# Kernel optimization log

Hardware: AMD Instinct MI355X
Metric: run time of the kernel (lower is better)

Reference implementation:

```python
import jax, jax.numpy as jnp
import numpy as np

H = 64
V = 50257
B = 32
L = 4096
LN_EPS = 1e-5
DELTA_EPS = 1e-6


def setup_inputs() -> dict:
    key = jax.random.key(0)
    ks = jax.random.split(key, 10)
    s = 0.02
    return {
        "seq": jax.random.randint(ks[0], (B, L), 0, V),
        "read_pos": -1,
        "embed": jax.random.normal(ks[1], (V, H), jnp.float32) * s,
        "w1": jax.random.normal(ks[2], (H, 2 * H), jnp.float32) * s,
        "b1": jnp.zeros((2 * H,), jnp.float32),
        "w2": jax.random.normal(ks[3], (2 * H, H), jnp.float32) * s,
        "b2": jnp.zeros((H,), jnp.float32),
        "ln_g": jnp.ones((H,), jnp.float32),
        "ln_b": jnp.zeros((H,), jnp.float32),
        "rp_w": jax.random.normal(ks[4], (H, H), jnp.float32) * s,
        "rp_b": jnp.zeros((H,), jnp.float32),
        "out_w": jax.random.normal(ks[5], (H, V), jnp.float32) * s,
        "out_b": jnp.zeros((V,), jnp.float32),
    }


def _encoder(seq, embed, w1, b1, w2, b2, ln_g, ln_b):
    e = embed[seq]  # [B, L, H]
    f = jnp.maximum(e @ w1 + b1, 0.0) @ w2 + b2  # FFN
    x = e + f
    mu = jnp.mean(x, axis=-1, keepdims=True)
    var = jnp.mean((x - mu) ** 2, axis=-1, keepdims=True)
    return (x - mu) * jax.lax.rsqrt(var + LN_EPS) * ln_g + ln_b


def _delta_memory(h_all):
    # Strictly sequential delta-rule fast-weight update over t = 0..L-2.
    Bs, Ls, Hs = h_all.shape
    keys = jnp.transpose(h_all[:, : Ls - 1, :], (1, 0, 2))  # [L-1, B, H]

    def step(M, k):
        vp = jnp.einsum('bij,bj->bi', M, k)  # M @ k
        u = k - vp / (jnp.sum(k * k, axis=-1, keepdims=True) + DELTA_EPS)
        M = M + u[:, :, None] * k[:, None, :]  # outer product update
        return M, None

    M0 = jnp.zeros((Bs, Hs, Hs), h_all.dtype)
    M, _ = jax.lax.scan(step, M0, keys)
    return M


def reference(seq, read_pos, embed, w1, b1, w2, b2, ln_g, ln_b, rp_w, rp_b, out_w, out_b):
    h_all = _encoder(seq, embed, w1, b1, w2, b2, ln_g, ln_b)  # [B, L, H]
    M = _delta_memory(h_all)  # [B, H, H]
    q = h_all[:, read_pos, :]  # [B, H]
    r = jnp.einsum('bij,bj->bi', M, q)
    return (r @ rp_w + rp_b) @ out_w + out_b  # [B, V]
```

## Files before the change

### kernel.cpp

```cpp
#include <hip/hip_runtime.h>

#define HH 64
#define VV 50257
#define BB 32
#define LL 4096

constexpr float LN_EPS_F = 1e-5f;
constexpr float DELTA_EPS_F = 1e-6f;

constexpr int CS = 64;
constexpr int NG = LL / CS;

typedef float f32x4 __attribute__((ext_vector_type(4)));
typedef float f32x2 __attribute__((ext_vector_type(2)));
typedef short bf16x8 __attribute__((ext_vector_type(8)));
union U16x8 { uint4 u; bf16x8 v; unsigned short s[8]; };

__device__ __forceinline__ unsigned short f2bf(float f) {
  union { float f; unsigned u; } v; v.f = f;
  unsigned r = v.u + 0x7fff + ((v.u >> 16) & 1);
  return (unsigned short)(r >> 16);
}

__device__ __forceinline__ unsigned cvt_pk_bf16(float a, float b) {
  unsigned r;
  asm("v_cvt_pk_bf16_f32 %0, %1, %2" : "=v"(r) : "v"(a), "v"(b));
  return r;
}

__device__ __forceinline__ void split2(float a, float b, unsigned& hp, unsigned& lp) {
  hp = cvt_pk_bf16(a, b);
  float ha = __uint_as_float(hp << 16);
  float hb = __uint_as_float(hp & 0xffff0000u);
  lp = cvt_pk_bf16(a - ha, b - hb);
}

template <int CTRL>
__device__ __forceinline__ float dpp_add(float x) {
  int t = __builtin_amdgcn_update_dpp(0, __float_as_int(x), CTRL, 0xF, 0xF, true);
  return x + __int_as_float(t);
}

__device__ __forceinline__ float wave_sum_lane63(float x) {
  x = dpp_add<0x111>(x);
  x = dpp_add<0x112>(x);
  x = dpp_add<0x114>(x);
  x = dpp_add<0x118>(x);
  x = dpp_add<0x142>(x);
  x = dpp_add<0x143>(x);
  return x;
}

__device__ __forceinline__ float readlane_f(float x, int lane) {
  return __int_as_float(__builtin_amdgcn_readlane(__float_as_int(x), lane));
}

__global__ __launch_bounds__(256) void prep_kernel(
    const float* __restrict__ w1, const float* __restrict__ w2,
    unsigned short* __restrict__ w1b, unsigned short* __restrict__ w2b) {
  int i = blockIdx.x * 256 + threadIdx.x;
  if (i < 8192) {
    int jj = i >> 6, h = i & 63;
    w1b[i] = f2bf(w1[h * 128 + jj]);
  } else {
    int k = i - 8192;
    int h = k >> 7, jj = k & 127;
    w2b[k] = f2bf(w2[jj * 64 + h]);
  }
}

__global__ __launch_bounds__(64, 1) void encoder_kernel(
    const int* __restrict__ seq, const float* __restrict__ embed,
    const unsigned short* __restrict__ w1b, const float* __restrict__ b1,
    const unsigned short* __restrict__ w2b, const float* __restrict__ b2,
    const float* __restrict__ ln_g, const float* __restrict__ ln_b,
    float* __restrict__ h_all, float* __restrict__ beta) {
  __shared__ __align__(16) char pool[16640];
  unsigned short (*e_l)[72] = reinterpret_cast<unsigned short (*)[72]>(pool);
  unsigned short (*chunk)[40] = reinterpret_cast<unsigned short (*)[40]>(pool + 9216);
  float (*x_l)[65] = reinterpret_cast<float (*)[65]>(pool);
  __shared__ float2 gb_l[64];
  __shared__ float b1_l[128], b2_l[64];

  int lane = threadIdx.x;
  int q = lane >> 4, l = lane & 15;
  int base = blockIdx.x * 64;
  int s = seq[base + lane];

  {
    const float4* ep = reinterpret_cast<const float4*>(embed + (size_t)s * HH);
#pragma unroll
    for (int i = 0; i < 8; ++i) {
      float4 va = ep[2 * i], vb = ep[2 * i + 1];
      uint4 u;
      u.x = cvt_pk_bf16(va.x, va.y);
      u.y = cvt_pk_bf16(va.z, va.w);
      u.z = cvt_pk_bf16(vb.x, vb.y);
      u.w = cvt_pk_bf16(vb.z, vb.w);
      *(uint4*)&e_l[lane][8 * i] = u;
    }
  }
  gb_l[lane] = make_float2(ln_g[lane], ln_b[lane]);
  b1_l[lane] = b1[lane];
  b1_l[64 + lane] = b1[64 + lane];
  b2_l[lane] = b2[lane];

  bf16x8 af1[8][2];
#pragma unroll
  for (int mi = 0; mi < 8; ++mi)
#pragma unroll
    for (int ks = 0; ks < 2; ++ks) {
      U16x8 t;
      t.u = *(const uint4*)(w1b + (mi * 16 + l) * 64 + ks * 32 + q * 8);
      af1[mi][ks] = t.v;
    }

  __syncthreads();

  f32x4 acc1[8][4];
#pragma unroll
  for (int mi = 0; mi < 8; ++mi)
#pragma unroll
    for (int nt = 0; nt < 4; ++nt) acc1[mi][nt] = (f32x4){0.f, 0.f, 0.f, 0.f};

#pragma unroll
  for (int ks = 0; ks < 2; ++ks) {
    bf16x8 bfr[4];
#pragma unroll
    for (int nt = 0; nt < 4; ++nt) {
      U16x8 t;
      t.u = *(const uint4*)&e_l[nt * 16 + l][ks * 32 + q * 8];
      bfr[nt] = t.v;
    }
#pragma unroll
    for (int mi = 0; mi < 8; ++mi)
#pragma unroll
      for (int nt = 0; nt < 4; ++nt)
        acc1[mi][nt] = __builtin_amdgcn_mfma_f32_16x16x32_bf16(
            af1[mi][ks], bfr[nt], acc1[mi][nt], 0, 0, 0);
  }

  bf16x8 bf2[4][4];
#pragma unroll
  for (int nt = 0; nt < 4; ++nt)
#pragma unroll
    for (int ks = 0; ks < 4; ++ks) {
      U16x8 t;
      t.u = *(const uint4*)(w2b + (nt * 16 + l) * 128 + ks * 32 + q * 8);
      bf2[nt][ks] = t.v;
    }

  f32x4 acc2[4][4];
#pragma unroll
  for (int mt = 0; mt < 4; ++mt)
#pragma unroll
    for (int nt = 0; nt < 4; ++nt) acc2[mt][nt] = (f32x4){0.f, 0.f, 0.f, 0.f};

#pragma unroll
  for (int ks2 = 0; ks2 < 4; ++ks2) {
#pragma unroll
    for (int mm = 0; mm < 2; ++mm) {
      int mi = 2 * ks2 + mm;
      int jj0 = mi * 16 + q * 4;
      int col = mm * 16 + q * 4;
#pragma unroll
      for (int nt = 0; nt < 4; ++nt) {
        int tok = nt * 16 + l;
        float v0 = fmaxf(acc1[mi][nt][0] + b1_l[jj0 + 0], 0.f);
        float v1 = fmaxf(acc1[mi][nt][1] + b1_l[jj0 + 1], 0.f);
        float v2 = fmaxf(acc1[mi][nt][2] + b1_l[jj0 + 2], 0.f);
        float v3 = fmaxf(acc1[mi][nt][3] + b1_l[jj0 + 3], 0.f);
        uint2 u;
        u.x = cvt_pk_bf16(v0, v1);
        u.y = cvt_pk_bf16(v2, v3);
        *(uint2*)&chunk[tok][col] = u;
      }
    }
    __syncthreads();

    bf16x8 afr[4];
#pragma unroll
    for (int mt = 0; mt < 4; ++mt) {
      U16x8 t;
      t.u = *(const uint4*)&chunk[mt * 16 + l][q * 8];
      afr[mt] = t.v;
    }
#pragma unroll
    for (int mt = 0; mt < 4; ++mt)
#pragma unroll
      for (int nt = 0; nt < 4; ++nt)
        acc2[mt][nt] = __builtin_amdgcn_mfma_f32_16x16x32_bf16(
            afr[mt], bf2[nt][ks2], acc2[mt][nt], 0, 0, 0);
    __syncthreads();
  }

#pragma unroll
  for (int mt = 0; mt < 4; ++mt)
#pragma unroll
    for (int nt = 0; nt < 4; ++nt) {
      int h = nt * 16 + l;
#pragma unroll
      for (int r = 0; r < 4; ++r) {
        int tok = mt * 16 + q * 4 + r;
        x_l[tok][h] = acc2[mt][nt][r] + b2_l[h];
      }
    }

  __syncthreads();

  float x[HH];
#pragma unroll
  for (int h = 0; h < HH; ++h) x[h] = x_l[lane][h];
  {
    const float4* ep = reinterpret_cast<const float4*>(embed + (size_t)s * HH);
#pragma unroll
    for (int i = 0; i < 16; ++i) {
      float4 v = ep[i];
      x[4 * i + 0] += v.x; x[4 * i + 1] += v.y;
      x[4 * i + 2] += v.z; x[4 * i + 3] += v.w;
    }
  }
  float sum = 0.f;
#pragma unroll
  for (int h = 0; h < HH; ++h) sum += x[h];
  float mu = sum * (1.f / HH);
  float vs = 0.f;
#pragma unroll
  for (int h = 0; h < HH; ++h) { float dx = x[h] - mu; vs = fmaf(dx, dx, vs); }
  float rstd = rsqrtf(vs * (1.f / HH) + LN_EPS_F);

  float ss = 0.f;
#pragma unroll
  for (int h = 0; h < HH; ++h) {
    float2 gb = gb_l[h];
    float o = fmaf((x[h] - mu) * rstd, gb.x, gb.y);
    ss = fmaf(o, o, ss);
    x[h] = o;
  }
  float4* hp = reinterpret_cast<float4*>(h_all + (size_t)(base + lane) * HH);
#pragma unroll
  for (int i = 0; i < 16; ++i)
    hp[i] = make_float4(x[4 * i + 0], x[4 * i + 1], x[4 * i + 2], x[4 * i + 3]);
  beta[base + lane] = 1.f / (ss + DELTA_EPS_F);
}

__global__ __launch_bounds__(64, 2) void gram_n_kernel(
    const float* __restrict__ h_all, const float* __restrict__ beta,
    float* __restrict__ Ng) {
  __shared__ __align__(16) char smem[8704];
  float* Glp = reinterpret_cast<float*>(smem);
  char* pBh0 = smem;
  float* bl = reinterpret_cast<float*>(smem + 8448);

  int c = blockIdx.x, b = blockIdx.y, lane = threadIdx.x;
  int q = lane >> 4, l = lane & 15;
  const float* src = h_all + ((size_t)b * LL + c * CS) * HH;

  bf16x8 ah[2][4], al_[2][4];
#pragma unroll
  for (int ks = 0; ks < 2; ++ks)
#pragma unroll
    for (int i = 0; i < 4; ++i) {
      const float* p = src + (i * 16 + l) * 64 + ks * 32 + q * 8;
      float4 va = *(const float4*)p, vb = *(const float4*)(p + 4);
      U16x8 hi, lo;
      split2(va.x, va.y, hi.u.x, lo.u.x);
      split2(va.z, va.w, hi.u.y, lo.u.y);
      split2(vb.x, vb.y, hi.u.z, lo.u.z);
      split2(vb.z, vb.w, hi.u.w, lo.u.w);
      ah[ks][i] = hi.v; al_[ks][i] = lo.v;
    }
  if (c == NG - 1 && l == 15) {
#pragma unroll
    for (int ks = 0; ks < 2; ++ks) {
      ah[ks][3] = (bf16x8){0, 0, 0, 0, 0, 0, 0, 0};
      al_[ks][3] = (bf16x8){0, 0, 0, 0, 0, 0, 0, 0};
    }
  }

  bl[lane] = beta[(size_t)b * LL + c * CS + lane];

  f32x2 m2[32];
#pragma unroll
  for (int t = 0; t < 32; ++t)
    m2[t] = (f32x2){src[(2 * t) * 64 + lane], src[(2 * t + 1) * 64 + lane]};
  if (c == NG - 1) m2[31].y = 0.f;

  f32x4 acc[4][4];
#pragma unroll
  for (int mi = 0; mi < 4; ++mi)
#pragma unroll
    for (int nt = 0; nt <= mi; ++nt) acc[mi][nt] = (f32x4){0.f, 0.f, 0.f, 0.f};

#pragma unroll
  for (int ks = 0; ks < 2; ++ks)
#pragma unroll
    for (int mi = 0; mi < 4; ++mi)
#pragma unroll
      for (int nt = 0; nt <= mi; ++nt) {
        acc[mi][nt] = __builtin_amdgcn_mfma_f32_16x16x32_bf16(ah[ks][mi], ah[ks][nt], acc[mi][nt], 0, 0, 0);
        acc[mi][nt] = __builtin_amdgcn_mfma_f32_16x16x32_bf16(ah[ks][mi], al_[ks][nt], acc[mi][nt], 0, 0, 0);
        acc[mi][nt] = __builtin_amdgcn_mfma_f32_16x16x32_bf16(al_[ks][mi], ah[ks][nt], acc[mi][nt], 0, 0, 0);
      }

#pragma unroll
  for (int mi = 0; mi < 4; ++mi) {
    int gg = 4 * mi + q;
    int e1 = 8 * gg * (gg + 1);
    int o0 = 4 * gg * (2 * gg + 1);
    int o1 = e1;
    int o2 = e1 + 4 * (gg + 1);
    int o3 = e1 + 8 * (gg + 1);
#pragma unroll
    for (int nt = 0; nt < mi; ++nt) {
      int t = nt * 16 + l;
      Glp[o0 + t] = acc[mi][nt][0];
      Glp[o1 + t] = acc[mi][nt][1];
      Glp[o2 + t] = acc[mi][nt][2];
      Glp[o3 + t] = acc[mi][nt][3];
    }
    {
      int t = mi * 16 + l;
      if (l < 4 * q)     Glp[o0 + t] = acc[mi][mi][0];
      if (l < 4 * q + 1) Glp[o1 + t] = acc[mi][mi][1];
      if (l < 4 * q + 2) Glp[o2 + t] = acc[mi][mi][2];
      if (l < 4 * q + 3) Glp[o3 + t] = acc[mi][mi][3];
    }
  }
  __syncthreads();

#pragma unroll
  for (int g = 15; g >= 0; --g) {
    int e1 = 8 * g * (g + 1);
    int o0 = 4 * g * (2 * g + 1);
    int o1 = e1;
    int o2 = e1 + 4 * (g + 1);
    int o3 = e1 + 8 * (g + 1);
    float4 C1 = *(const float4*)(Glp + o1 + 4 * g);
    float4 C2 = *(const float4*)(Glp + o2 + 4 * g);
    float4 C3 = *(const float4*)(Glp + o3 + 4 * g);
    float4 B4 = *(const float4*)(bl + 4 * g);

    float t3 = B4.w * m2[2 * g + 1].y;
    float v2 = fmaf(-C3.z, t3, m2[2 * g + 1].x);
    float t2 = B4.z * v2;
    float v1 = fmaf(-C2.y, t2, fmaf(-C3.y, t3, m2[2 * g].y));
    float t1 = B4.y * v1;
    float v0 = fmaf(-C1.x, t1, fmaf(-C2.x, t2, fmaf(-C3.x, t3, m2[2 * g].x)));
    float t0 = B4.x * v0;
    m2[2 * g] = (f32x2){t0, t1};
    m2[2 * g + 1] = (f32x2){t2, t3};
    f32x2 n0 = {-t0, -t0}, n1 = {-t1, -t1}, n2 = {-t2, -t2}, n3 = {-t3, -t3};

#pragma unroll
    for (int j = 0; j < g; ++j) {
      float4 R0 = *(const float4*)(Glp + o0 + 4 * j);
      float4 R1 = *(const float4*)(Glp + o1 + 4 * j);
      float4 R2 = *(const float4*)(Glp + o2 + 4 * j);
      float4 R3 = *(const float4*)(Glp + o3 + 4 * j);
      f32x2 a = m2[2 * j], d = m2[2 * j + 1];
      a = __builtin_elementwise_fma((f32x2){R0.x, R0.y}, n0, a);
      a = __builtin_elementwise_fma((f32x2){R1.x, R1.y}, n1, a);
      a = __builtin_elementwise_fma((f32x2){R2.x, R2.y}, n2, a);
      a = __builtin_elementwise_fma((f32x2){R3.x, R3.y}, n3, a);
      d = __builtin_elementwise_fma((f32x2){R0.z, R0.w}, n0, d);
      d = __builtin_elementwise_fma((f32x2){R1.z, R1.w}, n1, d);
      d = __builtin_elementwise_fma((f32x2){R2.z, R2.w}, n2, d);
      d = __builtin_elementwise_fma((f32x2){R3.z, R3.w}, n3, d);
      m2[2 * j] = a; m2[2 * j + 1] = d;
    }
  }

  __syncthreads();

  f32x4 acc2[4][4];
#pragma unroll
  for (int mi = 0; mi < 4; ++mi)
#pragma unroll
    for (int nt = 0; nt < 4; ++nt) acc2[mi][nt] = (f32x4){0.f, 0.f, 0.f, 0.f};

#pragma unroll
  for (int hf = 0; hf < 2; ++hf) {
    float av[4][8];
#pragma unroll
    for (int mi = 0; mi < 4; ++mi)
#pragma unroll
      for (int r = 0; r < 8; ++r)
        av[mi][r] = src[(hf * 32 + q * 8 + r) * 64 + mi * 16 + l];

#pragma unroll
    for (int i2 = 0; i2 < 8; ++i2) {
      int tt = hf * 16 + 2 * i2;
      unsigned h0, l0, h1, l1;
      split2(m2[tt].x, m2[tt].y, h0, l0);
      split2(m2[tt + 1].x, m2[tt + 1].y, h1, l1);
      unsigned boff = (unsigned)((lane * 64 + i2 * 8) ^ ((lane & 7) << 4));
      *(uint2*)(pBh0 + boff) = make_uint2(h0, h1);
      *(uint2*)(pBh0 + 4096 + boff) = make_uint2(l0, l1);
    }
    __syncthreads();

    if (c == NG - 1 && hf == 1 && q == 3) {
      av[0][7] = 0.f; av[1][7] = 0.f; av[2][7] = 0.f; av[3][7] = 0.f;
    }

    bf16x8 ka[4], kl2[4];
#pragma unroll
    for (int mi = 0; mi < 4; ++mi) {
      U16x8 hi, lo;
      split2(av[mi][0], av[mi][1], hi.u.x, lo.u.x);
      split2(av[mi][2], av[mi][3], hi.u.y, lo.u.y);
      split2(av[mi][4], av[mi][5], hi.u.z, lo.u.z);
      split2(av[mi][6], av[mi][7], hi.u.w, lo.u.w);
      ka[mi] = hi.v; kl2[mi] = lo.v;
    }

    bf16x8 bh[4], blo[4];
#pragma unroll
    for (int i = 0; i < 4; ++i) {
      unsigned bro = (unsigned)((((16 * i + l) * 64) + q * 16) ^ ((l & 7) << 4));
      U16x8 t;
      t.u = *(const uint4*)(pBh0 + bro);        bh[i] = t.v;
      t.u = *(const uint4*)(pBh0 + 4096 + bro); blo[i] = t.v;
    }

#pragma unroll
    for (int mi = 0; mi < 4; ++mi)
#pragma unroll
      for (int nt = 0; nt < 4; ++nt) {
        acc2[mi][nt] = __builtin_amdgcn_mfma_f32_16x16x32_bf16(ka[mi], bh[nt], acc2[mi][nt], 0, 0, 0);
        acc2[mi][nt] = __builtin_amdgcn_mfma_f32_16x16x32_bf16(ka[mi], blo[nt], acc2[mi][nt], 0, 0, 0);
        acc2[mi][nt] = __builtin_amdgcn_mfma_f32_16x16x32_bf16(kl2[mi], bh[nt], acc2[mi][nt], 0, 0, 0);
      }
    __syncthreads();
  }

  float* np = Ng + (((size_t)b * NG + c) << 12);
#pragma unroll
  for (int mi = 0; mi < 4; ++mi)
#pragma unroll
    for (int nt = 0; nt < 4; ++nt) {
      int h0 = mi * 16 + q * 4, hp = nt * 16 + l;
      float4 v;
      v.x = ((h0 + 0 == hp) ? 1.f : 0.f) - acc2[mi][nt][0];
      v.y = ((h0 + 1 == hp) ? 1.f : 0.f) - acc2[mi][nt][1];
      v.z = ((h0 + 2 == hp) ? 1.f : 0.f) - acc2[mi][nt][2];
      v.w = ((h0 + 3 == hp) ? 1.f : 0.f) - acc2[mi][nt][3];
      *(float4*)&np[hp * 64 + h0] = v;
    }
}

__global__ __launch_bounds__(64, 1) void boundary_kernel(
    const float* __restrict__ h_all, const float* __restrict__ Ng,
    const int* __restrict__ read_pos_p, float* __restrict__ Qg) {
  __shared__ __align__(16) float nt0[64 * 64];
  __shared__ __align__(16) float nt1[64 * 64];
  __shared__ __align__(16) float ql[64];

  int b = blockIdx.x, lane = threadIdx.x;
  int rpv = read_pos_p[0];
  int pos = rpv < 0 ? rpv + LL : rpv;
  float Q = h_all[((size_t)b * LL + pos) * HH + lane];

  const float* Nb = Ng + ((size_t)b * NG << 12);

  auto load_chunk = [&](float* buf, int c) {
    const float* g = Nb + ((size_t)c << 12);
#pragma unroll
    for (int i = 0; i < 16; ++i)
      __builtin_amdgcn_global_load_lds(
          (const __attribute__((address_space(1))) unsigned*)(g + i * 256 + lane * 4),
          (__attribute__((address_space(3))) unsigned*)(buf + i * 256), 16, 0, 0);
  };

  auto step = [&](const float* buf, int c, bool last) {
    if (last) __builtin_amdgcn_s_waitcnt(0x0F70);
    else      __builtin_amdgcn_s_waitcnt(0x4F70);
    Qg[((size_t)b * NG + c) * HH + lane] = Q;
    ql[lane] = Q;
    float a0 = 0.f, a1 = 0.f, a2 = 0.f, a3 = 0.f;
#pragma unroll
    for (int j = 0; j < 64; j += 4) {
      float4 q4 = *(const float4*)&ql[j];
      a0 = fmaf(buf[(j + 0) * 64 + lane], q4.x, a0);
      a1 = fmaf(buf[(j + 1) * 64 + lane], q4.y, a1);
      a2 = fmaf(buf[(j + 2) * 64 + lane], q4.z, a2);
      a3 = fmaf(buf[(j + 3) * 64 + lane], q4.w, a3);
    }
    Q = (a0 + a1) + (a2 + a3);
  };

  load_chunk(nt1, NG - 1);
  load_chunk(nt0, NG - 2);

#pragma unroll 1
  for (int c = NG - 1; c >= 1; c -= 2) {
    step(nt1, c, false);
    __builtin_amdgcn_s_waitcnt(0xC07F);
    if (c >= 3) load_chunk(nt1, c - 2);
    step(nt0, c - 1, c == 1);
    __builtin_amdgcn_s_waitcnt(0xC07F);
    if (c >= 3) load_chunk(nt0, c - 3);
  }
}

__global__ __launch_bounds__(64, 1) void chunk_scan_kernel(
    const float* __restrict__ h_all, const float* __restrict__ beta,
    const float* __restrict__ Qg, float* __restrict__ rc) {
  int c = blockIdx.x, b = blockIdx.y, j = threadIdx.x;
  const float* hb = h_all + (size_t)b * LL * HH;
  const float* betab = beta + (size_t)b * LL;

  float P = Qg[((size_t)b * NG + c) * HH + j];
  float r = 0.f;

  float kk[CS];
#pragma unroll
  for (int i = 0; i < CS; ++i) kk[i] = hb[((size_t)(c * CS + i)) * HH + j];
  float bv = betab[c * CS + j];

  bool last = (c == NG - 1);
#pragma unroll
  for (int i = CS - 1; i >= 0; --i) {
    float k = kk[i];
    float bt = readlane_f(bv, i);
    float m = k * P;
    float s = wave_sum_lane63(m);
    float d = readlane_f(s, 63);
    if (i == CS - 1 && last) d = 0.f;
    r = fmaf(d, k, r);
    P = fmaf(-(bt * d), k, P);
  }
  rc[((size_t)b * NG + c) * HH + j] = r;
}

__global__ __launch_bounds__(64, 1) void combine_kernel(
    const float* __restrict__ rc, const float* __restrict__ rp_w,
    const float* __restrict__ rp_b, float* __restrict__ yv) {
  int b = blockIdx.x, j = threadIdx.x;
  float r = 0.f;
#pragma unroll 8
  for (int cc = 0; cc < NG; ++cc) r += rc[((size_t)b * NG + cc) * HH + j];
  __shared__ float rs[HH];
  rs[j] = r;
  __syncthreads();
  float yj = rp_b[j];
#pragma unroll
  for (int h = 0; h < HH; ++h) yj = fmaf(rs[h], rp_w[h * HH + j], yj);
  yv[b * HH + j] = yj;
}

__global__ __launch_bounds__(256, 2) void out_kernel(
    const float* __restrict__ yv, const float* __restrict__ out_w,
    const float* __restrict__ out_b, float* __restrict__ out) {
  __shared__ float ys[BB * HH];
  for (int i = threadIdx.x; i < BB * HH; i += 256) ys[i] = yv[i];
  __syncthreads();

  int v = blockIdx.x * 256 + threadIdx.x;
  if (v >= VV) return;

  float acc[BB];
  float ob = out_b[v];
#pragma unroll
  for (int b = 0; b < BB; ++b) acc[b] = ob;

  for (int h = 0; h < HH; ++h) {
    float w = out_w[(size_t)h * VV + v];
#pragma unroll
    for (int b = 0; b < BB; ++b) acc[b] = fmaf(ys[b * HH + h], w, acc[b]);
  }
#pragma unroll
  for (int b = 0; b < BB; ++b) out[(size_t)b * VV + v] = acc[b];
}

extern "C" void kernel_launch(void* const* d_in, const int* in_sizes, int n_in,
                              void* d_out, int out_size, void* d_ws, size_t ws_size,
                              hipStream_t stream) {
  (void)in_sizes; (void)n_in; (void)out_size; (void)ws_size;
  const int*   seq   = (const int*)d_in[0];
  const int*   rp    = (const int*)d_in[1];
  const float* embed = (const float*)d_in[2];
  const float* w1    = (const float*)d_in[3];
  const float* b1    = (const float*)d_in[4];
  const float* w2    = (const float*)d_in[5];
  const float* b2    = (const float*)d_in[6];
  const float* ln_g  = (const float*)d_in[7];
  const float* ln_b  = (const float*)d_in[8];
  const float* rp_w  = (const float*)d_in[9];
  const float* rp_b  = (const float*)d_in[10];
  const float* out_w = (const float*)d_in[11];
  const float* out_b = (const float*)d_in[12];
  float* out = (float*)d_out;

  float* h_all = (float*)d_ws;
  float* beta  = h_all + (size_t)BB * LL * HH;
  float* Ng    = beta + (size_t)BB * LL;
  float* Qg    = Ng + (size_t)BB * NG * HH * HH;
  float* rcv   = Qg + (size_t)BB * NG * HH;
  float* yv    = rcv + (size_t)BB * NG * HH;
  unsigned short* w1b = (unsigned short*)(yv + (size_t)BB * HH);
  unsigned short* w2b = w1b + 8192;

  prep_kernel<<<64, 256, 0, stream>>>(w1, w2, w1b, w2b);
  encoder_kernel<<<BB * LL / 64, 64, 0, stream>>>(seq, embed, w1b, b1, w2b, b2,
                                                  ln_g, ln_b, h_all, beta);
  gram_n_kernel<<<dim3(NG, BB), 64, 0, stream>>>(h_all, beta, Ng);
  boundary_kernel<<<BB, 64, 0, stream>>>(h_all, Ng, rp, Qg);
  chunk_scan_kernel<<<dim3(NG, BB), 64, 0, stream>>>(h_all, beta, Qg, rcv);
  combine_kernel<<<BB, 64, 0, stream>>>(rcv, rp_w, rp_b, yv);
  out_kernel<<<(VV + 255) / 256, 256, 0, stream>>>(yv, out_w, out_b, out);
}
```

Before: 221.3 us.

## Split encoder FFN into halves for occupancy; deepen boundary prefetch to four buffers

The encoder kernel now computes the first FFN matmul in two halves of 64 hidden units, interleaving each half with its share of the second matmul. This shrinks live accumulator and weight registers enough to allow two waves per SIMD (launch_bounds 64,2). The boundary kernel's sequential chunk propagation moves from double to quadruple buffering of the 16 KB N matrices via async global-to-LDS loads, with graded vmcnt waits, to hide more load latency on the serial critical path. The cost is more LDS per block and reloading w2 fragments per step.

```diff
diff --git a/kernel.cpp b/kernel.cpp
--- a/kernel.cpp
+++ b/kernel.cpp
@@ -69,7 +69,7 @@
   }
 }
 
-__global__ __launch_bounds__(64, 1) void encoder_kernel(
+__global__ __launch_bounds__(64, 2) void encoder_kernel(
     const int* __restrict__ seq, const float* __restrict__ embed,
     const unsigned short* __restrict__ w1b, const float* __restrict__ b1,
     const unsigned short* __restrict__ w2b, const float* __restrict__ b2,
@@ -105,93 +105,94 @@
   b1_l[64 + lane] = b1[64 + lane];
   b2_l[lane] = b2[lane];
 
-  bf16x8 af1[8][2];
-#pragma unroll
-  for (int mi = 0; mi < 8; ++mi)
+  __syncthreads();
+
+  f32x4 acc2[4][4];
+#pragma unroll
+  for (int mt = 0; mt < 4; ++mt)
+#pragma unroll
+    for (int nt = 0; nt < 4; ++nt) acc2[mt][nt] = (f32x4){0.f, 0.f, 0.f, 0.f};
+
+#pragma unroll
+  for (int half = 0; half < 2; ++half) {
+    bf16x8 af1[4][2];
+#pragma unroll
+    for (int mi2 = 0; mi2 < 4; ++mi2)
+#pragma unroll
+      for (int ks = 0; ks < 2; ++ks) {
+        U16x8 t;
+        t.u = *(const uint4*)(w1b + ((half * 4 + mi2) * 16 + l) * 64 + ks * 32 + q * 8);
+        af1[mi2][ks] = t.v;
+      }
+
+    f32x4 acc1[4][4];
+#pragma unroll
+    for (int mi2 = 0; mi2 < 4; ++mi2)
+#pragma unroll
+      for (int nt = 0; nt < 4; ++nt) acc1[mi2][nt] = (f32x4){0.f, 0.f, 0.f, 0.f};
+
 #pragma unroll
     for (int ks = 0; ks < 2; ++ks) {
-      U16x8 t;
-      t.u = *(const uint4*)(w1b + (mi * 16 + l) * 64 + ks * 32 + q * 8);
-      af1[mi][ks] = t.v;
-    }
-
-  __syncthreads();
-
-  f32x4 acc1[8][4];
-#pragma unroll
-  for (int mi = 0; mi < 8; ++mi)
-#pragma unroll
-    for (int nt = 0; nt < 4; ++nt) acc1[mi][nt] = (f32x4){0.f, 0.f, 0.f, 0.f};
-
-#pragma unroll
-  for (int ks = 0; ks < 2; ++ks) {
-    bf16x8 bfr[4];
-#pragma unroll
-    for (int nt = 0; nt < 4; ++nt) {
-      U16x8 t;
-      t.u = *(const uint4*)&e_l[nt * 16 + l][ks * 32 + q * 8];
-      bfr[nt] = t.v;
-    }
-#pragma unroll
-    for (int mi = 0; mi < 8; ++mi)
-#pragma unroll
-      for (int nt = 0; nt < 4; ++nt)
-        acc1[mi][nt] = __builtin_amdgcn_mfma_f32_16x16x32_bf16(
-            af1[mi][ks], bfr[nt], acc1[mi][nt], 0, 0, 0);
-  }
-
-  bf16x8 bf2[4][4];
-#pragma unroll
-  for (int nt = 0; nt < 4; ++nt)
-#pragma unroll
-    for (int ks = 0; ks < 4; ++ks) {
-      U16x8 t;
-      t.u = *(const uint4*)(w2b + (nt * 16 + l) * 128 + ks * 32 + q * 8);
-      bf2[nt][ks] = t.v;
-    }
-
-  f32x4 acc2[4][4];
-#pragma unroll
-  for (int mt = 0; mt < 4; ++mt)
-#pragma unroll
-    for (int nt = 0; nt < 4; ++nt) acc2[mt][nt] = (f32x4){0.f, 0.f, 0.f, 0.f};
-
-#pragma unroll
-  for (int ks2 = 0; ks2 < 4; ++ks2) {
-#pragma unroll
-    for (int mm = 0; mm < 2; ++mm) {
-      int mi = 2 * ks2 + mm;
-      int jj0 = mi * 16 + q * 4;
-      int col = mm * 16 + q * 4;
+      bf16x8 bfr[4];
 #pragma unroll
       for (int nt = 0; nt < 4; ++nt) {
-        int tok = nt * 16 + l;
-        float v0 = fmaxf(acc1[mi][nt][0] + b1_l[jj0 + 0], 0.f);
-        float v1 = fmaxf(acc1[mi][nt][1] + b1_l[jj0 + 1], 0.f);
-        float v2 = fmaxf(acc1[mi][nt][2] + b1_l[jj0 + 2], 0.f);
-        float v3 = fmaxf(acc1[mi][nt][3] + b1_l[jj0 + 3], 0.f);
-        uint2 u;
-        u.x = cvt_pk_bf16(v0, v1);
-        u.y = cvt_pk_bf16(v2, v3);
-        *(uint2*)&chunk[tok][col] = u;
-      }
-    }
-    __syncthreads();
-
-    bf16x8 afr[4];
-#pragma unroll
-    for (int mt = 0; mt < 4; ++mt) {
-      U16x8 t;
-      t.u = *(const uint4*)&chunk[mt * 16 + l][q * 8];
-      afr[mt] = t.v;
-    }
-#pragma unroll
-    for (int mt = 0; mt < 4; ++mt)
-#pragma unroll
-      for (int nt = 0; nt < 4; ++nt)
-        acc2[mt][nt] = __builtin_amdgcn_mfma_f32_16x16x32_bf16(
-            afr[mt], bf2[nt][ks2], acc2[mt][nt], 0, 0, 0);
-    __syncthreads();
+        U16x8 t;
+        t.u = *(const uint4*)&e_l[nt * 16 + l][ks * 32 + q * 8];
+        bfr[nt] = t.v;
+      }
+#pragma unroll
+      for (int mi2 = 0; mi2 < 4; ++mi2)
+#pragma unroll
+        for (int nt = 0; nt < 4; ++nt)
+          acc1[mi2][nt] = __builtin_amdgcn_mfma_f32_16x16x32_bf16(
+              af1[mi2][ks], bfr[nt], acc1[mi2][nt], 0, 0, 0);
+    }
+
+#pragma unroll
+    for (int kk2 = 0; kk2 < 2; ++kk2) {
+      int ks2 = half * 2 + kk2;
+#pragma unroll
+      for (int mm = 0; mm < 2; ++mm) {
+        int mi2 = 2 * kk2 + mm;
+        int jj0 = (half * 4 + mi2) * 16 + q * 4;
+        int col = mm * 16 + q * 4;
+#pragma unroll
+        for (int nt = 0; nt < 4; ++nt) {
+          int tok = nt * 16 + l;
+          float v0 = fmaxf(acc1[mi2][nt][0] + b1_l[jj0 + 0], 0.f);
+          float v1 = fmaxf(acc1[mi2][nt][1] + b1_l[jj0 + 1], 0.f);
+          float v2 = fmaxf(acc1[mi2][nt][2] + b1_l[jj0 + 2], 0.f);
+          float v3 = fmaxf(acc1[mi2][nt][3] + b1_l[jj0 + 3], 0.f);
+          uint2 u;
+          u.x = cvt_pk_bf16(v0, v1);
+          u.y = cvt_pk_bf16(v2, v3);
+          *(uint2*)&chunk[tok][col] = u;
+        }
+      }
+      __syncthreads();
+
+      bf16x8 bf2s[4];
+#pragma unroll
+      for (int nt = 0; nt < 4; ++nt) {
+        U16x8 t;
+        t.u = *(const uint4*)(w2b + (nt * 16 + l) * 128 + ks2 * 32 + q * 8);
+        bf2s[nt] = t.v;
+      }
+      bf16x8 afr[4];
+#pragma unroll
+      for (int mt = 0; mt < 4; ++mt) {
+        U16x8 t;
+        t.u = *(const uint4*)&chunk[mt * 16 + l][q * 8];
+        afr[mt] = t.v;
+      }
+#pragma unroll
+      for (int mt = 0; mt < 4; ++mt)
+#pragma unroll
+        for (int nt = 0; nt < 4; ++nt)
+          acc2[mt][nt] = __builtin_amdgcn_mfma_f32_16x16x32_bf16(
+              afr[mt], bf2s[nt], acc2[mt][nt], 0, 0, 0);
+      __syncthreads();
+    }
   }
 
 #pragma unroll
@@ -453,9 +454,8 @@
 __global__ __launch_bounds__(64, 1) void boundary_kernel(
     const float* __restrict__ h_all, const float* __restrict__ Ng,
     const int* __restrict__ read_pos_p, float* __restrict__ Qg) {
-  __shared__ __align__(16) float nt0[64 * 64];
-  __shared__ __align__(16) float nt1[64 * 64];
-  __shared__ __align__(16) float ql[64];
+  __shared__ __align__(16) float nt[4][4096];
+  __shared__ float ql[64];
 
   int b = blockIdx.x, lane = threadIdx.x;
   int rpv = read_pos_p[0];
@@ -473,9 +473,19 @@
           (__attribute__((address_space(3))) unsigned*)(buf + i * 256), 16, 0, 0);
   };
 
-  auto step = [&](const float* buf, int c, bool last) {
-    if (last) __builtin_amdgcn_s_waitcnt(0x0F70);
-    else      __builtin_amdgcn_s_waitcnt(0x4F70);
+  load_chunk(nt[0], NG - 1);
+  load_chunk(nt[1], NG - 2);
+  load_chunk(nt[2], NG - 3);
+  load_chunk(nt[3], NG - 4);
+
+#pragma unroll 1
+  for (int c = NG - 1; c >= 1; --c) {
+    if (c >= 4)      __builtin_amdgcn_s_waitcnt(0xCF70);
+    else if (c == 3) __builtin_amdgcn_s_waitcnt(0x8F70);
+    else if (c == 2) __builtin_amdgcn_s_waitcnt(0x4F70);
+    else             __builtin_amdgcn_s_waitcnt(0x0F70);
+
+    const float* buf = nt[(NG - 1 - c) & 3];
     Qg[((size_t)b * NG + c) * HH + lane] = Q;
     ql[lane] = Q;
     float a0 = 0.f, a1 = 0.f, a2 = 0.f, a3 = 0.f;
@@ -488,20 +498,11 @@
       a3 = fmaf(buf[(j + 3) * 64 + lane], q4.w, a3);
     }
     Q = (a0 + a1) + (a2 + a3);
-  };
-
-  load_chunk(nt1, NG - 1);
-  load_chunk(nt0, NG - 2);
-
-#pragma unroll 1
-  for (int c = NG - 1; c >= 1; c -= 2) {
-    step(nt1, c, false);
+
     __builtin_amdgcn_s_waitcnt(0xC07F);
-    if (c >= 3) load_chunk(nt1, c - 2);
-    step(nt0, c - 1, c == 1);
-    __builtin_amdgcn_s_waitcnt(0xC07F);
-    if (c >= 3) load_chunk(nt0, c - 3);
-  }
+    if (c >= 5) load_chunk(nt[(NG - 1 - c) & 3], c - 4);
+  }
+  Qg[((size_t)b * NG + 0) * HH + lane] = Q;
 }
 
 __global__ __launch_bounds__(64, 1) void chunk_scan_kernel(
```

After: 223.3 us. No clear change (+0.9%).

## Split boundary scan matvec across four waves with deeper prefetch pipeline

Applied to the files above, without the earlier changes.

The boundary kernel grows from one wave to four per batch. Each wave computes a quarter of the 64x64 matrix-vector product and the partial sums are reduced through shared memory. Chunk loads are spread across the waves and the prefetch depth goes from two buffers to four. The goal is to shorten the serial per-chunk latency of the backward scan and hide more of the global load latency, at the cost of two block barriers per step.

```diff
diff --git a/kernel.cpp b/kernel.cpp
--- a/kernel.cpp
+++ b/kernel.cpp
@@ -450,58 +450,70 @@
     }
 }
 
-__global__ __launch_bounds__(64, 1) void boundary_kernel(
+__global__ __launch_bounds__(256, 1) void boundary_kernel(
     const float* __restrict__ h_all, const float* __restrict__ Ng,
     const int* __restrict__ read_pos_p, float* __restrict__ Qg) {
-  __shared__ __align__(16) float nt0[64 * 64];
-  __shared__ __align__(16) float nt1[64 * 64];
-  __shared__ __align__(16) float ql[64];
-
-  int b = blockIdx.x, lane = threadIdx.x;
+  __shared__ __align__(16) float nt[4][4096];
+  __shared__ float ql[64];
+  __shared__ float ps[4][64];
+
+  int b = blockIdx.x, tid = threadIdx.x;
+  int w = tid >> 6, h = tid & 63;
   int rpv = read_pos_p[0];
   int pos = rpv < 0 ? rpv + LL : rpv;
-  float Q = h_all[((size_t)b * LL + pos) * HH + lane];
+  float Q = h_all[((size_t)b * LL + pos) * HH + h];
 
   const float* Nb = Ng + ((size_t)b * NG << 12);
 
-  auto load_chunk = [&](float* buf, int c) {
+  auto load_quarter = [&](float* buf, int c) {
     const float* g = Nb + ((size_t)c << 12);
 #pragma unroll
-    for (int i = 0; i < 16; ++i)
+    for (int k = 0; k < 4; ++k) {
+      int i = 4 * w + k;
       __builtin_amdgcn_global_load_lds(
-          (const __attribute__((address_space(1))) unsigned*)(g + i * 256 + lane * 4),
+          (const __attribute__((address_space(1))) unsigned*)(g + i * 256 + h * 4),
           (__attribute__((address_space(3))) unsigned*)(buf + i * 256), 16, 0, 0);
+    }
   };
 
-  auto step = [&](const float* buf, int c, bool last) {
-    if (last) __builtin_amdgcn_s_waitcnt(0x0F70);
-    else      __builtin_amdgcn_s_waitcnt(0x4F70);
-    Qg[((size_t)b * NG + c) * HH + lane] = Q;
-    ql[lane] = Q;
+  if (w == 0) ql[h] = Q;
+  load_quarter(nt[0], NG - 1);
+  load_quarter(nt[1], NG - 2);
+  load_quarter(nt[2], NG - 3);
+  load_quarter(nt[3], NG - 4);
+
+#pragma unroll 1
+  for (int c = NG - 1; c >= 1; --c) {
+    if (c >= 4)      __builtin_amdgcn_s_waitcnt(0x007C);
+    else if (c == 3) __builtin_amdgcn_s_waitcnt(0x0078);
+    else if (c == 2) __builtin_amdgcn_s_waitcnt(0x0074);
+    else             __builtin_amdgcn_s_waitcnt(0x0070);
+    __builtin_amdgcn_s_barrier();
+
+    if (w == 0) Qg[((size_t)b * NG + c) * HH + h] = Q;
+
+    const float* buf = nt[(NG - 1 - c) & 3];
     float a0 = 0.f, a1 = 0.f, a2 = 0.f, a3 = 0.f;
 #pragma unroll
-    for (int j = 0; j < 64; j += 4) {
+    for (int jj = 0; jj < 4; ++jj) {
+      int j = 16 * w + 4 * jj;
       float4 q4 = *(const float4*)&ql[j];
-      a0 = fmaf(buf[(j + 0) * 64 + lane], q4.x, a0);
-      a1 = fmaf(buf[(j + 1) * 64 + lane], q4.y, a1);
-      a2 = fmaf(buf[(j + 2) * 64 + lane], q4.z, a2);
-      a3 = fmaf(buf[(j + 3) * 64 + lane], q4.w, a3);
-    }
-    Q = (a0 + a1) + (a2 + a3);
-  };
-
-  load_chunk(nt1, NG - 1);
-  load_chunk(nt0, NG - 2);
-
-#pragma unroll 1
-  for (int c = NG - 1; c >= 1; c -= 2) {
-    step(nt1, c, false);
+      a0 = fmaf(buf[(j + 0) * 64 + h], q4.x, a0);
+      a1 = fmaf(buf[(j + 1) * 64 + h], q4.y, a1);
+      a2 = fmaf(buf[(j + 2) * 64 + h], q4.z, a2);
+      a3 = fmaf(buf[(j + 3) * 64 + h], q4.w, a3);
+    }
+    ps[w][h] = (a0 + a1) + (a2 + a3);
     __builtin_amdgcn_s_waitcnt(0xC07F);
-    if (c >= 3) load_chunk(nt1, c - 2);
-    step(nt0, c - 1, c == 1);
-    __builtin_amdgcn_s_waitcnt(0xC07F);
-    if (c >= 3) load_chunk(nt0, c - 3);
-  }
+    __builtin_amdgcn_s_barrier();
+
+    if (w == 0) {
+      Q = (ps[0][h] + ps[1][h]) + (ps[2][h] + ps[3][h]);
+      ql[h] = Q;
+    }
+    if (c >= 5) load_quarter(nt[(NG - 1 - c) & 3], c - 4);
+  }
+  if (w == 0) Qg[(size_t)b * NG * HH + h] = Q;
 }
 
 __global__ __launch_bounds__(64, 1) void chunk_scan_kernel(
@@ -606,7 +618,7 @@
   encoder_kernel<<<BB * LL / 64, 64, 0, stream>>>(seq, embed, w1b, b1, w2b, b2,
                                                   ln_g, ln_b, h_all, beta);
   gram_n_kernel<<<dim3(NG, BB), 64, 0, stream>>>(h_all, beta, Ng);
-  boundary_kernel<<<BB, 64, 0, stream>>>(h_all, Ng, rp, Qg);
+  boundary_kernel<<<BB, 256, 0, stream>>>(h_all, Ng, rp, Qg);
   chunk_scan_kernel<<<dim3(NG, BB), 64, 0, stream>>>(h_all, beta, Qg, rcv);
   combine_kernel<<<BB, 64, 0, stream>>>(rcv, rp_w, rp_b, yv);
   out_kernel<<<(VV + 255) / 256, 256, 0, stream>>>(yv, out_w, out_b, out);
```

New measurement: 224.9 us. Within noise of the previous version (+1.6%).

## Split sequential boundary chain into segment products, short chain, and parallel segment sweeps

Applied to the files above, without the earlier changes.

Replaces the single per-batch boundary kernel, which walked all 64 chunk transition matrices serially, with a three-stage hierarchical scan. The first stage multiplies 8 chunk matrices per segment in parallel using split-bf16 MFMA. The second runs a short 7-step chain over segment products to get segment boundary vectors. The third propagates within each segment in parallel. This shortens the serial dependency chain from 64 steps to about 7+7, at the cost of two extra launches, extra workspace, and the rounding error of the bf16 hi/lo split (three MFMAs, dropping the lo*lo term) in the segment products.

```diff
diff --git a/kernel.cpp b/kernel.cpp
--- a/kernel.cpp
+++ b/kernel.cpp
@@ -10,6 +10,8 @@
 
 constexpr int CS = 64;
 constexpr int NG = LL / CS;
+constexpr int SEG = 8;
+constexpr int NS = NG / SEG;
 
 typedef float f32x4 __attribute__((ext_vector_type(4)));
 typedef float f32x2 __attribute__((ext_vector_type(2)));
@@ -450,22 +452,112 @@
     }
 }
 
-__global__ __launch_bounds__(64, 1) void boundary_kernel(
-    const float* __restrict__ h_all, const float* __restrict__ Ng,
-    const int* __restrict__ read_pos_p, float* __restrict__ Qg) {
-  __shared__ __align__(16) float nt0[64 * 64];
-  __shared__ __align__(16) float nt1[64 * 64];
-  __shared__ __align__(16) float ql[64];
-
+__global__ __launch_bounds__(64, 1) void segprod_kernel(
+    const float* __restrict__ Ng, float* __restrict__ Mg) {
+  __shared__ __align__(16) float Tst[64 * 76];
+  int s = blockIdx.x, b = blockIdx.y, lane = threadIdx.x;
+  int q = lane >> 4, l = lane & 15;
+  const float* base = Ng + (((size_t)b * NG + s * SEG) << 12);
+
+#pragma unroll
+  for (int j = 0; j < 64; ++j) Tst[lane * 76 + j] = (j == lane) ? 1.f : 0.f;
+
+  f32x4 bufA[2][16];
+  auto loadA = [&](f32x4* dst, int c) {
+#pragma unroll
+    for (int ks = 0; ks < 2; ++ks)
+#pragma unroll
+      for (int i = 0; i < 4; ++i) {
+        const float* p = base + ((size_t)c << 12) + (i * 16 + l) * 64 + ks * 32 + q * 8;
+        dst[(ks * 4 + i) * 2 + 0] = *(const f32x4*)p;
+        dst[(ks * 4 + i) * 2 + 1] = *(const f32x4*)(p + 4);
+      }
+  };
+  loadA(bufA[0], 0);
+
+  f32x4 acc[4][4];
+#pragma unroll
+  for (int c = 0; c < SEG; ++c) {
+    if (c < SEG - 1) loadA(bufA[(c + 1) & 1], c + 1);
+
+    bf16x8 ah[2][4], al_[2][4];
+#pragma unroll
+    for (int ks = 0; ks < 2; ++ks)
+#pragma unroll
+      for (int i = 0; i < 4; ++i) {
+        f32x4 va = bufA[c & 1][(ks * 4 + i) * 2 + 0];
+        f32x4 vb = bufA[c & 1][(ks * 4 + i) * 2 + 1];
+        U16x8 hi, lo;
+        split2(va[0], va[1], hi.u.x, lo.u.x);
+        split2(va[2], va[3], hi.u.y, lo.u.y);
+        split2(vb[0], vb[1], hi.u.z, lo.u.z);
+        split2(vb[2], vb[3], hi.u.w, lo.u.w);
+        ah[ks][i] = hi.v; al_[ks][i] = lo.v;
+      }
+    bf16x8 bh[2][4], bl_[2][4];
+#pragma unroll
+    for (int ks = 0; ks < 2; ++ks)
+#pragma unroll
+      for (int i = 0; i < 4; ++i) {
+        const float* p = &Tst[(i * 16 + l) * 76 + ks * 32 + q * 8];
+        f32x4 va = *(const f32x4*)p, vb = *(const f32x4*)(p + 4);
+        U16x8 hi, lo;
+        split2(va[0], va[1], hi.u.x, lo.u.x);
+        split2(va[2], va[3], hi.u.y, lo.u.y);
+        split2(vb[0], vb[1], hi.u.z, lo.u.z);
+        split2(vb[2], vb[3], hi.u.w, lo.u.w);
+        bh[ks][i] = hi.v; bl_[ks][i] = lo.v;
+      }
+
+#pragma unroll
+    for (int mi = 0; mi < 4; ++mi)
+#pragma unroll
+      for (int nt = 0; nt < 4; ++nt) acc[mi][nt] = (f32x4){0.f, 0.f, 0.f, 0.f};
+
+#pragma unroll
+    for (int ks = 0; ks < 2; ++ks)
+#pragma unroll
+      for (int mi = 0; mi < 4; ++mi)
+#pragma unroll
+        for (int nt = 0; nt < 4; ++nt) {
+          acc[mi][nt] = __builtin_amdgcn_mfma_f32_16x16x32_bf16(ah[ks][mi], bh[ks][nt], acc[mi][nt], 0, 0, 0);
+          acc[mi][nt] = __builtin_amdgcn_mfma_f32_16x16x32_bf16(ah[ks][mi], bl_[ks][nt], acc[mi][nt], 0, 0, 0);
+          acc[mi][nt] = __builtin_amdgcn_mfma_f32_16x16x32_bf16(al_[ks][mi], bh[ks][nt], acc[mi][nt], 0, 0, 0);
+        }
+
+    if (c < SEG - 1) {
+#pragma unroll
+      for (int mi = 0; mi < 4; ++mi)
+#pragma unroll
+        for (int nt = 0; nt < 4; ++nt)
+#pragma unroll
+          for (int r = 0; r < 4; ++r)
+            Tst[(nt * 16 + l) * 76 + mi * 16 + q * 4 + r] = acc[mi][nt][r];
+    }
+  }
+  float* mp = Mg + (((size_t)b * NS + s) << 12);
+#pragma unroll
+  for (int mi = 0; mi < 4; ++mi)
+#pragma unroll
+    for (int nt = 0; nt < 4; ++nt)
+#pragma unroll
+      for (int r = 0; r < 4; ++r)
+        mp[(mi * 16 + q * 4 + r) * 64 + nt * 16 + l] = acc[mi][nt][r];
+}
+
+__global__ __launch_bounds__(64, 1) void segchain_kernel(
+    const float* __restrict__ h_all, const float* __restrict__ Mg,
+    const int* __restrict__ read_pos_p, float* __restrict__ Bg) {
+  __shared__ __align__(16) float nt0[4096], nt1[4096];
+  __shared__ float ql[64];
   int b = blockIdx.x, lane = threadIdx.x;
   int rpv = read_pos_p[0];
   int pos = rpv < 0 ? rpv + LL : rpv;
   float Q = h_all[((size_t)b * LL + pos) * HH + lane];
-
-  const float* Nb = Ng + ((size_t)b * NG << 12);
-
-  auto load_chunk = [&](float* buf, int c) {
-    const float* g = Nb + ((size_t)c << 12);
+  const float* Mb = Mg + ((size_t)b * NS << 12);
+
+  auto load_chunk = [&](float* buf, int s) {
+    const float* g = Mb + ((size_t)s << 12);
 #pragma unroll
     for (int i = 0; i < 16; ++i)
       __builtin_amdgcn_global_load_lds(
@@ -473,11 +565,16 @@
           (__attribute__((address_space(3))) unsigned*)(buf + i * 256), 16, 0, 0);
   };
 
-  auto step = [&](const float* buf, int c, bool last) {
-    if (last) __builtin_amdgcn_s_waitcnt(0x0F70);
-    else      __builtin_amdgcn_s_waitcnt(0x4F70);
-    Qg[((size_t)b * NG + c) * HH + lane] = Q;
+  Bg[(b * NS + 7) * HH + lane] = Q;
+  load_chunk(nt0, 7);
+  load_chunk(nt1, 6);
+
+#pragma unroll 1
+  for (int k = 0; k < 7; ++k) {
+    if (k < 6) __builtin_amdgcn_s_waitcnt(0x4F70);
+    else       __builtin_amdgcn_s_waitcnt(0x0F70);
     ql[lane] = Q;
+    const float* buf = (k & 1) ? nt1 : nt0;
     float a0 = 0.f, a1 = 0.f, a2 = 0.f, a3 = 0.f;
 #pragma unroll
     for (int j = 0; j < 64; j += 4) {
@@ -488,20 +585,55 @@
       a3 = fmaf(buf[(j + 3) * 64 + lane], q4.w, a3);
     }
     Q = (a0 + a1) + (a2 + a3);
+    Bg[(b * NS + 6 - k) * HH + lane] = Q;
+    __builtin_amdgcn_s_waitcnt(0xC07F);
+    if (k + 2 <= 6) load_chunk((k & 1) ? nt1 : nt0, 5 - k);
+  }
+}
+
+__global__ __launch_bounds__(64, 1) void segqg_kernel(
+    const float* __restrict__ Ng, const float* __restrict__ Bg,
+    float* __restrict__ Qg) {
+  __shared__ __align__(16) float nt0[4096], nt1[4096];
+  __shared__ float ql[64];
+  int s = blockIdx.x, b = blockIdx.y, lane = threadIdx.x;
+  float Q = Bg[(b * NS + s) * HH + lane];
+  const float* Nb = Ng + (((size_t)b * NG + s * SEG) << 12);
+
+  auto load_chunk = [&](float* buf, int ci) {
+    const float* g = Nb + ((size_t)ci << 12);
+#pragma unroll
+    for (int i = 0; i < 16; ++i)
+      __builtin_amdgcn_global_load_lds(
+          (const __attribute__((address_space(1))) unsigned*)(g + i * 256 + lane * 4),
+          (__attribute__((address_space(3))) unsigned*)(buf + i * 256), 16, 0, 0);
   };
 
-  load_chunk(nt1, NG - 1);
-  load_chunk(nt0, NG - 2);
+  load_chunk(nt0, 7);
+  load_chunk(nt1, 6);
 
 #pragma unroll 1
-  for (int c = NG - 1; c >= 1; c -= 2) {
-    step(nt1, c, false);
+  for (int k = 0; k < 7; ++k) {
+    if (k < 6) __builtin_amdgcn_s_waitcnt(0x4F70);
+    else       __builtin_amdgcn_s_waitcnt(0x0F70);
+    int c = s * SEG + 7 - k;
+    Qg[((size_t)b * NG + c) * HH + lane] = Q;
+    ql[lane] = Q;
+    const float* buf = (k & 1) ? nt1 : nt0;
+    float a0 = 0.f, a1 = 0.f, a2 = 0.f, a3 = 0.f;
+#pragma unroll
+    for (int j = 0; j < 64; j += 4) {
+      float4 q4 = *(const float4*)&ql[j];
+      a0 = fmaf(buf[(j + 0) * 64 + lane], q4.x, a0);
+      a1 = fmaf(buf[(j + 1) * 64 + lane], q4.y, a1);
+      a2 = fmaf(buf[(j + 2) * 64 + lane], q4.z, a2);
+      a3 = fmaf(buf[(j + 3) * 64 + lane], q4.w, a3);
+    }
+    Q = (a0 + a1) + (a2 + a3);
     __builtin_amdgcn_s_waitcnt(0xC07F);
-    if (c >= 3) load_chunk(nt1, c - 2);
-    step(nt0, c - 1, c == 1);
-    __builtin_amdgcn_s_waitcnt(0xC07F);
-    if (c >= 3) load_chunk(nt0, c - 3);
-  }
+    if (k + 2 <= 6) load_chunk((k & 1) ? nt1 : nt0, 5 - k);
+  }
+  Qg[((size_t)b * NG + s * SEG) * HH + lane] = Q;
 }
 
 __global__ __launch_bounds__(64, 1) void chunk_scan_kernel(
@@ -601,12 +733,16 @@
   float* yv    = rcv + (size_t)BB * NG * HH;
   unsigned short* w1b = (unsigned short*)(yv + (size_t)BB * HH);
   unsigned short* w2b = w1b + 8192;
+  float* Mg = (float*)(w2b + 8192);
+  float* Bg = Mg + (size_t)BB * NS * HH * HH;
 
   prep_kernel<<<64, 256, 0, stream>>>(w1, w2, w1b, w2b);
   encoder_kernel<<<BB * LL / 64, 64, 0, stream>>>(seq, embed, w1b, b1, w2b, b2,
                                                   ln_g, ln_b, h_all, beta);
   gram_n_kernel<<<dim3(NG, BB), 64, 0, stream>>>(h_all, beta, Ng);
-  boundary_kernel<<<BB, 64, 0, stream>>>(h_all, Ng, rp, Qg);
+  segprod_kernel<<<dim3(NS, BB), 64, 0, stream>>>(Ng, Mg);
+  segchain_kernel<<<BB, 64, 0, stream>>>(h_all, Mg, rp, Bg);
+  segqg_kernel<<<dim3(NS, BB), 64, 0, stream>>>(Ng, Bg, Qg);
   chunk_scan_kernel<<<dim3(NG, BB), 64, 0, stream>>>(h_all, beta, Qg, rcv);
   combine_kernel<<<BB, 64, 0, stream>>>(rcv, rp_w, rp_b, yv);
   out_kernel<<<(VV + 255) / 256, 256, 0, stream>>>(yv, out_w, out_b, out);
```

New measurement: 233.1 us. 1.05x slower.
